# Performance work log

Hardware: AMD Instinct MI355X
Metric: run time of the kernel (lower is better)

The kernel has to match this reference:

```python
import jax, jax.numpy as jnp
import numpy as np

N = 50000
E = 800000
F_IN = 128
H = 128
C = 16


def _balanced_conv(x, row, col, W, b, num_nodes):
    # x: [N, in] -> linear -> gather(row) * norm -> scatter-add(col) + bias
    x = x @ W  # [N, out]
    deg = jax.ops.segment_sum(jnp.ones(row.shape[0], x.dtype), col,
                              num_segments=num_nodes)  # includes self-loops -> deg >= 1
    dinv = deg ** -0.5
    norm = dinv[row] * dinv[col]  # [E+N]
    msg = norm[:, None] * x[row]  # gather + scale
    out = jax.ops.segment_sum(msg, col, num_segments=num_nodes)  # scatter-add
    return out + b


def setup_inputs() -> dict:
    key = jax.random.key(0)
    ks = jax.random.split(key, 12)
    x = jax.random.normal(ks[0], (N, F_IN), dtype=jnp.float32)
    edge_index = jax.random.randint(ks[1], (2, E), 0, N, dtype=jnp.int64)
    s = 1.0 / np.sqrt(F_IN)
    sh = 1.0 / np.sqrt(H)
    return {
        "x": x,
        "edge_index": edge_index,
        "importance": jnp.ones((F_IN,), jnp.float32),
        "W1": jax.random.uniform(ks[2], (F_IN, H), jnp.float32, -s, s),
        "b1": jnp.zeros((H,), jnp.float32),
        "W2": jax.random.uniform(ks[3], (H, H), jnp.float32, -sh, sh),
        "b2": jnp.zeros((H,), jnp.float32),
        "W3": jax.random.uniform(ks[4], (H, H), jnp.float32, -sh, sh),
        "b3": jnp.zeros((H,), jnp.float32),
        "lw1": jax.random.uniform(ks[5], (H, H), jnp.float32, -sh, sh),
        "lb1": jax.random.uniform(ks[6], (H,), jnp.float32, -sh, sh),
        "lw2": jax.random.uniform(ks[7], (H, C), jnp.float32, -sh, sh),
        "lb2": jax.random.uniform(ks[8], (C,), jnp.float32, -sh, sh),
    }


def reference(x, edge_index, importance, W1, b1, W2, b2, W3, b3, lw1, lb1, lw2, lb2):
    num_nodes = x.shape[0]
    # add self-loops (static shape: E + N)
    loops = jnp.arange(num_nodes, dtype=edge_index.dtype)
    row = jnp.concatenate([edge_index[0], loops])
    col = jnp.concatenate([edge_index[1], loops])

    gelu = lambda t: jax.nn.gelu(t, approximate=False)  # torch F.gelu default = erf

    h = x * importance  # FeatureImportance
    h = gelu(_balanced_conv(h, row, col, W1, b1, num_nodes))
    h = gelu(_balanced_conv(h, row, col, W2, b2, num_nodes))
    h = gelu(_balanced_conv(h, row, col, W3, b3, num_nodes))
    h = gelu(h @ lw1 + lb1)
    return h @ lw2 + lb2  # [N, C]
```

## Files before the change

### kernel.cpp

```cpp
#include <hip/hip_runtime.h>
#include <math.h>

#define NNODES 50000
#define NEDGES 800000
#define FDIM 128
#define NBUCKET 196
#define BCAP 6144
#define ABLK 261
#define EPWA 3072
#define MGRID 782

typedef unsigned short ushortT;
typedef unsigned int uintT;
typedef __attribute__((ext_vector_type(8))) short short8;
typedef __attribute__((ext_vector_type(4))) float floatx4;

__device__ __forceinline__ float gelu_erf(float x){
    return 0.5f * x * (1.0f + erff(x * 0.70710678118654752f));
}
__device__ __forceinline__ float bflo(uintT u){ return __uint_as_float(u << 16); }
__device__ __forceinline__ float bfhi(uintT u){ return __uint_as_float(u & 0xFFFF0000u); }
__device__ __forceinline__ ushortT f2bf(float f){
    uintT u = __float_as_uint(f);
    return (ushortT)((u + 0x7FFFu + ((u >> 16) & 1u)) >> 16);
}
__device__ __forceinline__ void split_bf16(float f, ushortT& hi, ushortT& lo){
    uintT u = __float_as_uint(f);
    hi = (ushortT)(u >> 16);
    float fhi = __uint_as_float(u & 0xFFFF0000u);
    lo = (ushortT)(__float_as_uint(f - fhi) >> 16);
}

__global__ __launch_bounds__(256) void k_packW(const float* __restrict__ Wa,
                                               const float* __restrict__ Wb,
                                               const float* __restrict__ Wc,
                                               const float* __restrict__ Wd,
                                               const float* __restrict__ We,
                                               ushortT* __restrict__ Wp,
                                               int* __restrict__ gcur){
    int l = blockIdx.x;
    int t = threadIdx.x;
    if (l < 4){
        const float* W = (l==0) ? Wa : (l==1) ? Wb : (l==2) ? Wc : Wd;
        ushortT* hiP = Wp + (size_t)l*2*16384;
        ushortT* loP = hiP + 16384;
        for (int idx = t; idx < 16384; idx += 256){
            int k = idx >> 7, n = idx & 127;
            ushortT hi, lo;
            split_bf16(W[idx], hi, lo);
            int kc = k >> 5, quad = (k >> 3) & 3, j = k & 7;
            int nt = n >> 4, lane = (n & 15) + (quad << 4);
            int off = ((kc*8 + nt)*64 + lane)*8 + j;
            hiP[off] = hi;
            loP[off] = lo;
        }
    } else {
        if (t < NBUCKET) gcur[t] = 0;
        ushortT* hiP = Wp + (size_t)4*2*16384;
        ushortT* loP = hiP + 2048;
        for (int idx = t; idx < 2048; idx += 256){
            int k = idx >> 4, n = idx & 15;
            ushortT hi, lo;
            split_bf16(We[idx], hi, lo);
            int kc = k >> 5, quad = (k >> 3) & 3, j = k & 7;
            int lane = n + (quad << 4);
            int off = (kc*64 + lane)*8 + j;
            hiP[off] = hi;
            loP[off] = lo;
        }
    }
}

__global__ __launch_bounds__(256) void k_bucketA(const int* __restrict__ ei,
                                                 int* __restrict__ gcur,
                                                 uintT* __restrict__ bucket){
    __shared__ int hist[NBUCKET];
    __shared__ int base[NBUCKET];
    int t = threadIdx.x;
    if (t < NBUCKET) hist[t] = 0;
    __syncthreads();
    int e0 = blockIdx.x * EPWA;
    int cr_c[12], cr_r[12];
    #pragma unroll
    for (int p = 0; p < 12; p++){
        int e = e0 + p*256 + t;
        if (e < NEDGES){
            cr_r[p] = ei[e];
            cr_c[p] = ei[NEDGES + e];
            atomicAdd(&hist[cr_c[p] >> 8], 1);
        } else cr_c[p] = -1;
    }
    __syncthreads();
    if (t < NBUCKET){
        base[t] = atomicAdd(&gcur[t], hist[t]);
        hist[t] = 0;
    }
    __syncthreads();
    #pragma unroll
    for (int p = 0; p < 12; p++){
        int c = cr_c[p];
        if (c >= 0){
            int b = c >> 8;
            int lp = atomicAdd(&hist[b], 1);
            bucket[(size_t)b*BCAP + base[b] + lp] = ((uintT)c << 16) | (uintT)cr_r[p];
        }
    }
}

__global__ __launch_bounds__(256) void k_bucketB(const int* __restrict__ gcur,
                                                 const uintT* __restrict__ bucket,
                                                 int* __restrict__ offs,
                                                 float* __restrict__ dinv,
                                                 ushortT* __restrict__ csr2){
    __shared__ int sm[256];
    __shared__ int hist[256];
    __shared__ int lcur[256];
    int b = blockIdx.x;
    int t = threadIdx.x;
    int n0 = b << 8;

    int gv = (t < NBUCKET) ? gcur[t] : 0;
    sm[t] = gv;
    __syncthreads();
    for (int off = 1; off < 256; off <<= 1){
        int tv = (t >= off) ? sm[t-off] : 0;
        __syncthreads();
        sm[t] += tv;
        __syncthreads();
    }
    __shared__ int bbase_s;
    if (t == b) bbase_s = sm[t] - gv;
    hist[t] = 0;
    __syncthreads();
    int bbase = bbase_s;
    int count = gcur[b];
    const uintT* src = bucket + (size_t)b*BCAP;

    for (int i = t; i < count; i += 256)
        atomicAdd(&hist[(src[i] >> 16) & 255], 1);
    __syncthreads();

    int v = hist[t];
    sm[t] = v;
    __syncthreads();
    for (int off = 1; off < 256; off <<= 1){
        int tv = (t >= off) ? sm[t-off] : 0;
        __syncthreads();
        sm[t] += tv;
        __syncthreads();
    }
    int excl = bbase + sm[t] - v;
    int node = n0 + t;
    if (node <= NNODES) offs[node] = excl;
    if (node < NNODES) dinv[node] = rsqrtf((float)(v + 1));
    if (b == NBUCKET-1 && t == 255) offs[NNODES] = NEDGES;
    lcur[t] = excl;
    __syncthreads();

    for (int i = t; i < count; i += 256){
        uintT e = src[i];
        int pos = atomicAdd(&lcur[(e >> 16) & 255], 1);
        csr2[pos] = (ushortT)(e & 0xFFFFu);
    }
}

__global__ __launch_bounds__(256) void k_mfma_f32(const float* __restrict__ A,
                                                  const ushortT* __restrict__ Wp,
                                                  const float* __restrict__ scale,
                                                  const float* __restrict__ dinv,
                                                  ushortT* __restrict__ Yb){
    __shared__ float As[64*132];
    int t = threadIdx.x;
    int wave = t >> 6, lane = t & 63;
    int r = lane & 15, quad = lane >> 4;
    int row0 = blockIdx.x*64;
    int m0 = row0 + wave*16;
    const ushortT* WpLo = Wp + 16384;

    #pragma unroll
    for (int p = 0; p < 8; p++){
        int idx = p*256 + t;
        int rr = idx >> 5;
        int c4 = idx & 31;
        int gr = row0 + rr;
        float4 v = make_float4(0.f,0.f,0.f,0.f);
        if (gr < NNODES) v = *(const float4*)&A[(size_t)gr*FDIM + c4*4];
        float4 s = *(const float4*)&scale[c4*4];
        v.x*=s.x; v.y*=s.y; v.z*=s.z; v.w*=s.w;
        *(float4*)&As[rr*132 + c4*4] = v;
    }
    __syncthreads();

    floatx4 acc[8];
    #pragma unroll
    for (int nt = 0; nt < 8; nt++) acc[nt] = (floatx4){0.f,0.f,0.f,0.f};

    int arl = wave*16 + r;
    #pragma unroll
    for (int kc = 0; kc < 4; kc++){
        int kb = kc*32 + quad*8;
        float4 a0 = *(const float4*)&As[arl*132 + kb];
        float4 a1 = *(const float4*)&As[arl*132 + kb + 4];
        float av[8] = {a0.x, a0.y, a0.z, a0.w, a1.x, a1.y, a1.z, a1.w};
        short8 ahi, alo;
        #pragma unroll
        for (int e = 0; e < 8; e++){
            ushortT h, l;
            split_bf16(av[e], h, l);
            ahi[e] = (short)h;
            alo[e] = (short)l;
        }
        #pragma unroll
        for (int nt = 0; nt < 8; nt++){
            size_t boff = (size_t)(((kc*8 + nt)*64 + lane))*8;
            short8 bhi = *(const short8*)&Wp[boff];
            short8 blo = *(const short8*)&WpLo[boff];
            acc[nt] = __builtin_amdgcn_mfma_f32_16x16x32_bf16(ahi, bhi, acc[nt], 0, 0, 0);
            acc[nt] = __builtin_amdgcn_mfma_f32_16x16x32_bf16(alo, bhi, acc[nt], 0, 0, 0);
            acc[nt] = __builtin_amdgcn_mfma_f32_16x16x32_bf16(ahi, blo, acc[nt], 0, 0, 0);
        }
    }

    int orow0 = m0 + quad*4;
    float4 dv = *(const float4*)&dinv[orow0];
    float dva[4] = {dv.x, dv.y, dv.z, dv.w};
    #pragma unroll
    for (int nt = 0; nt < 8; nt++){
        int n = nt*16 + r;
        int chunk = n >> 6, o = n & 63;
        #pragma unroll
        for (int reg = 0; reg < 4; reg++){
            int orow = orow0 + reg;
            if (orow < NNODES){
                float v = acc[nt][reg] * dva[reg];
                Yb[((size_t)chunk*NNODES + orow)*64 + o] = f2bf(v);
            }
        }
    }
}

__global__ __launch_bounds__(256) void k_mfma_b16(const ushortT* __restrict__ Ab,
                                                  const ushortT* __restrict__ Wp,
                                                  const float* __restrict__ dinv,
                                                  ushortT* __restrict__ Yb){
    int t = threadIdx.x;
    int wave = t >> 6, lane = t & 63;
    int r = lane & 15, quad = lane >> 4;
    int m0 = blockIdx.x*64 + wave*16;
    int arow = m0 + r;
    if (arow >= NNODES) arow = NNODES - 1;
    const ushortT* WpLo = Wp + 16384;

    floatx4 acc[8];
    #pragma unroll
    for (int nt = 0; nt < 8; nt++) acc[nt] = (floatx4){0.f,0.f,0.f,0.f};

    short8 afr[4];
    #pragma unroll
    for (int kc = 0; kc < 4; kc++)
        afr[kc] = *(const short8*)&Ab[(size_t)arow*FDIM + kc*32 + quad*8];

    #pragma unroll
    for (int kc = 0; kc < 4; kc++){
        #pragma unroll
        for (int nt = 0; nt < 8; nt++){
            size_t boff = (size_t)(((kc*8 + nt)*64 + lane))*8;
            short8 bhi = *(const short8*)&Wp[boff];
            short8 blo = *(const short8*)&WpLo[boff];
            acc[nt] = __builtin_amdgcn_mfma_f32_16x16x32_bf16(afr[kc], bhi, acc[nt], 0, 0, 0);
            acc[nt] = __builtin_amdgcn_mfma_f32_16x16x32_bf16(afr[kc], blo, acc[nt], 0, 0, 0);
        }
    }

    int orow0 = m0 + quad*4;
    float4 dv = *(const float4*)&dinv[orow0];
    float dva[4] = {dv.x, dv.y, dv.z, dv.w};
    #pragma unroll
    for (int nt = 0; nt < 8; nt++){
        int n = nt*16 + r;
        int chunk = n >> 6, o = n & 63;
        #pragma unroll
        for (int reg = 0; reg < 4; reg++){
            int orow = orow0 + reg;
            if (orow < NNODES){
                float v = acc[nt][reg] * dva[reg];
                Yb[((size_t)chunk*NNODES + orow)*64 + o] = f2bf(v);
            }
        }
    }
}

__global__ __launch_bounds__(256) void k_mfma_final(const ushortT* __restrict__ Ab,
                                                    const ushortT* __restrict__ Wp1,
                                                    const ushortT* __restrict__ Wp2,
                                                    const float* __restrict__ lb1,
                                                    const float* __restrict__ lb2,
                                                    float* __restrict__ out){
    __shared__ ushortT Ls[64*136];
    int t = threadIdx.x;
    int wave = t >> 6, lane = t & 63;
    int r = lane & 15, quad = lane >> 4;
    int row0 = blockIdx.x*64;
    int m0 = row0 + wave*16;
    int arow = m0 + r;
    if (arow >= NNODES) arow = NNODES - 1;
    const ushortT* Wp1Lo = Wp1 + 16384;
    const ushortT* Wp2Lo = Wp2 + 2048;

    floatx4 acc[8];
    #pragma unroll
    for (int nt = 0; nt < 8; nt++) acc[nt] = (floatx4){0.f,0.f,0.f,0.f};

    short8 afr[4];
    #pragma unroll
    for (int kc = 0; kc < 4; kc++)
        afr[kc] = *(const short8*)&Ab[(size_t)arow*FDIM + kc*32 + quad*8];

    #pragma unroll
    for (int kc = 0; kc < 4; kc++){
        #pragma unroll
        for (int nt = 0; nt < 8; nt++){
            size_t boff = (size_t)(((kc*8 + nt)*64 + lane))*8;
            short8 bhi = *(const short8*)&Wp1[boff];
            short8 blo = *(const short8*)&Wp1Lo[boff];
            acc[nt] = __builtin_amdgcn_mfma_f32_16x16x32_bf16(afr[kc], bhi, acc[nt], 0, 0, 0);
            acc[nt] = __builtin_amdgcn_mfma_f32_16x16x32_bf16(afr[kc], blo, acc[nt], 0, 0, 0);
        }
    }

    int lrow0 = wave*16 + quad*4;
    #pragma unroll
    for (int nt = 0; nt < 8; nt++){
        int n = nt*16 + r;
        float bv = lb1[n];
        #pragma unroll
        for (int reg = 0; reg < 4; reg++){
            Ls[(lrow0 + reg)*136 + n] = f2bf(gelu_erf(acc[nt][reg] + bv));
        }
    }
    __syncthreads();

    floatx4 acc2 = (floatx4){0.f,0.f,0.f,0.f};
    #pragma unroll
    for (int kc = 0; kc < 4; kc++){
        short8 a2 = *(const short8*)&Ls[(wave*16 + r)*136 + kc*32 + quad*8];
        short8 bhi = *(const short8*)&Wp2[(size_t)(kc*64 + lane)*8];
        short8 blo = *(const short8*)&Wp2Lo[(size_t)(kc*64 + lane)*8];
        acc2 = __builtin_amdgcn_mfma_f32_16x16x32_bf16(a2, bhi, acc2, 0, 0, 0);
        acc2 = __builtin_amdgcn_mfma_f32_16x16x32_bf16(a2, blo, acc2, 0, 0, 0);
    }
    float bv2 = lb2[r];
    #pragma unroll
    for (int reg = 0; reg < 4; reg++){
        int orow = m0 + quad*4 + reg;
        if (orow < NNODES)
            out[(size_t)orow*16 + r] = acc2[reg] + bv2;
    }
}

__global__ __launch_bounds__(256) void k_aggregate(const ushortT* __restrict__ Yt,
                                                   const float* __restrict__ dinv,
                                                   const int* __restrict__ offs,
                                                   const ushortT* __restrict__ csr2,
                                                   const float* __restrict__ bias,
                                                   ushortT* __restrict__ Hout){
    int bid = blockIdx.x;
    int chunk = bid & 1;
    int node = (bid >> 1) * 8 + (threadIdx.x >> 5);
    int lane = threadIdx.x & 31;
    const uintT* Yc = (const uintT*)Yt + (size_t)chunk * NNODES * 32;

    uintT a0 = Yc[node*32 + lane];
    float2 acc;
    acc.x = bflo(a0);
    acc.y = bfhi(a0);
    int e0 = offs[node], e1 = offs[node+1];
    int e = e0;
    for (; e + 7 < e1; e += 8){
        int r0 = csr2[e+0];
        int r1 = csr2[e+1];
        int r2 = csr2[e+2];
        int r3 = csr2[e+3];
        int r4 = csr2[e+4];
        int r5 = csr2[e+5];
        int r6 = csr2[e+6];
        int r7 = csr2[e+7];
        uintT q0 = Yc[r0*32 + lane];
        uintT q1 = Yc[r1*32 + lane];
        uintT q2 = Yc[r2*32 + lane];
        uintT q3 = Yc[r3*32 + lane];
        uintT q4 = Yc[r4*32 + lane];
        uintT q5 = Yc[r5*32 + lane];
        uintT q6 = Yc[r6*32 + lane];
        uintT q7 = Yc[r7*32 + lane];
        acc.x += bflo(q0); acc.y += bfhi(q0);
        acc.x += bflo(q1); acc.y += bfhi(q1);
        acc.x += bflo(q2); acc.y += bfhi(q2);
        acc.x += bflo(q3); acc.y += bfhi(q3);
        acc.x += bflo(q4); acc.y += bfhi(q4);
        acc.x += bflo(q5); acc.y += bfhi(q5);
        acc.x += bflo(q6); acc.y += bfhi(q6);
        acc.x += bflo(q7); acc.y += bfhi(q7);
    }
    for (; e + 1 < e1; e += 2){
        int r0 = csr2[e], r1 = csr2[e+1];
        uintT q0 = Yc[r0*32 + lane];
        uintT q1 = Yc[r1*32 + lane];
        acc.x += bflo(q0); acc.y += bfhi(q0);
        acc.x += bflo(q1); acc.y += bfhi(q1);
    }
    if (e < e1){
        uintT q = Yc[csr2[e]*32 + lane];
        acc.x += bflo(q); acc.y += bfhi(q);
    }
    float dc = dinv[node];
    float2 bv = ((const float2*)bias)[chunk*32 + lane];
    acc.x = gelu_erf(fmaf(dc, acc.x, bv.x));
    acc.y = gelu_erf(fmaf(dc, acc.y, bv.y));
    uintT packed = (uintT)f2bf(acc.x) | ((uintT)f2bf(acc.y) << 16);
    *(uintT*)&Hout[(size_t)node*FDIM + chunk*64 + lane*2] = packed;
}

extern "C" void kernel_launch(void* const* d_in, const int* in_sizes, int n_in,
                              void* d_out, int out_size, void* d_ws, size_t ws_size,
                              hipStream_t stream) {
    const float* x    = (const float*)d_in[0];
    const int*   ei   = (const int*)d_in[1];
    const float* imp  = (const float*)d_in[2];
    const float* W1   = (const float*)d_in[3];
    const float* b1   = (const float*)d_in[4];
    const float* W2   = (const float*)d_in[5];
    const float* b2   = (const float*)d_in[6];
    const float* W3   = (const float*)d_in[7];
    const float* b3   = (const float*)d_in[8];
    const float* lw1  = (const float*)d_in[9];
    const float* lb1  = (const float*)d_in[10];
    const float* lw2  = (const float*)d_in[11];
    const float* lb2  = (const float*)d_in[12];
    float* out = (float*)d_out;

    int*   offs   = (int*)d_ws;
    int*   gcur   = (int*)d_ws + 50048;
    float* dinv   = (float*)d_ws + 50304;
    ushortT* csr2 = (ushortT*)((int*)d_ws + 100480);
    uintT* bucket = (uintT*)((int*)d_ws + 500480);
    ushortT* Wp   = (ushortT*)((int*)d_ws + 1704704);
    ushortT* bufYt= (ushortT*)((int*)d_ws + 1772544);
    ushortT* bufH = (ushortT*)((int*)d_ws + 4972544);

    dim3 B(256);
    k_packW  <<<5, B, 0, stream>>>(W1, W2, W3, lw1, lw2, Wp, gcur);
    k_bucketA<<<ABLK, B, 0, stream>>>(ei, gcur, bucket);
    k_bucketB<<<NBUCKET, B, 0, stream>>>(gcur, bucket, offs, dinv, csr2);

    k_mfma_f32 <<<MGRID, B, 0, stream>>>(x, Wp + 0*32768, imp, dinv, bufYt);
    k_aggregate<<<(NNODES/8)*2, B, 0, stream>>>(bufYt, dinv, offs, csr2, b1, bufH);
    k_mfma_b16 <<<MGRID, B, 0, stream>>>(bufH, Wp + 1*32768, dinv, bufYt);
    k_aggregate<<<(NNODES/8)*2, B, 0, stream>>>(bufYt, dinv, offs, csr2, b2, bufH);
    k_mfma_b16 <<<MGRID, B, 0, stream>>>(bufH, Wp + 2*32768, dinv, bufYt);
    k_aggregate<<<(NNODES/8)*2, B, 0, stream>>>(bufYt, dinv, offs, csr2, b3, bufH);

    k_mfma_final<<<MGRID, B, 0, stream>>>(bufH, Wp + 3*32768, Wp + 4*32768, lb1, lb2, out);
}
```

Before: 318.5 us.

## Fuse neighbor aggregation with following GEMM via shared-memory tile, row-major Y layout

Merges each aggregation kernel with the next layer's MFMA GEMM (and the final MLP). Each block aggregates 64 nodes into LDS and then multiplies from LDS. The intermediate Y layout changes from two 64-column chunks to full row-major 128 columns, so one wave gathers a full 256-byte row per edge. This removes the H round trip through global memory and three launches. In exchange, each block runs only 4 waves with a 16-node serial loop per wave, which lowers parallelism for the latency-bound gather and worsens load imbalance on degree skew.

```diff
diff --git a/kernel.cpp b/kernel.cpp
--- a/kernel.cpp
+++ b/kernel.cpp
@@ -164,6 +164,69 @@
     }
 }
 
+__device__ __forceinline__ void agg_phase(const uintT* __restrict__ Y2,
+                                          const float* __restrict__ dinv,
+                                          const int* __restrict__ offs,
+                                          const ushortT* __restrict__ csr2,
+                                          const float* __restrict__ bias,
+                                          uintT* __restrict__ Hs, int row0,
+                                          int wave, int lane){
+    float2 bv = ((const float2*)bias)[lane];
+    for (int g = 0; g < 16; g++){
+        int lrow = (g << 2) + wave;
+        int node = row0 + lrow;
+        float2 acc = make_float2(0.f, 0.f);
+        float dc = 0.f;
+        if (node < NNODES){
+            dc = dinv[node];
+            uintT a0 = Y2[(size_t)node*64 + lane];
+            acc.x = bflo(a0); acc.y = bfhi(a0);
+            int e0 = offs[node], e1 = offs[node+1];
+            int e = e0;
+            for (; e + 7 < e1; e += 8){
+                int s0 = csr2[e+0];
+                int s1 = csr2[e+1];
+                int s2 = csr2[e+2];
+                int s3 = csr2[e+3];
+                int s4 = csr2[e+4];
+                int s5 = csr2[e+5];
+                int s6 = csr2[e+6];
+                int s7 = csr2[e+7];
+                uintT q0 = Y2[(size_t)s0*64 + lane];
+                uintT q1 = Y2[(size_t)s1*64 + lane];
+                uintT q2 = Y2[(size_t)s2*64 + lane];
+                uintT q3 = Y2[(size_t)s3*64 + lane];
+                uintT q4 = Y2[(size_t)s4*64 + lane];
+                uintT q5 = Y2[(size_t)s5*64 + lane];
+                uintT q6 = Y2[(size_t)s6*64 + lane];
+                uintT q7 = Y2[(size_t)s7*64 + lane];
+                acc.x += bflo(q0); acc.y += bfhi(q0);
+                acc.x += bflo(q1); acc.y += bfhi(q1);
+                acc.x += bflo(q2); acc.y += bfhi(q2);
+                acc.x += bflo(q3); acc.y += bfhi(q3);
+                acc.x += bflo(q4); acc.y += bfhi(q4);
+                acc.x += bflo(q5); acc.y += bfhi(q5);
+                acc.x += bflo(q6); acc.y += bfhi(q6);
+                acc.x += bflo(q7); acc.y += bfhi(q7);
+            }
+            for (; e + 1 < e1; e += 2){
+                int s0 = csr2[e], s1 = csr2[e+1];
+                uintT q0 = Y2[(size_t)s0*64 + lane];
+                uintT q1 = Y2[(size_t)s1*64 + lane];
+                acc.x += bflo(q0); acc.y += bfhi(q0);
+                acc.x += bflo(q1); acc.y += bfhi(q1);
+            }
+            if (e < e1){
+                uintT q = Y2[(size_t)csr2[e]*64 + lane];
+                acc.x += bflo(q); acc.y += bfhi(q);
+            }
+        }
+        float ox = gelu_erf(fmaf(dc, acc.x, bv.x));
+        float oy = gelu_erf(fmaf(dc, acc.y, bv.y));
+        Hs[lrow*66 + lane] = (uintT)f2bf(ox) | ((uintT)f2bf(oy) << 16);
+    }
+}
+
 __global__ __launch_bounds__(256) void k_mfma_f32(const float* __restrict__ A,
                                                   const ushortT* __restrict__ Wp,
                                                   const float* __restrict__ scale,
@@ -227,39 +290,41 @@
     #pragma unroll
     for (int nt = 0; nt < 8; nt++){
         int n = nt*16 + r;
-        int chunk = n >> 6, o = n & 63;
         #pragma unroll
         for (int reg = 0; reg < 4; reg++){
             int orow = orow0 + reg;
-            if (orow < NNODES){
-                float v = acc[nt][reg] * dva[reg];
-                Yb[((size_t)chunk*NNODES + orow)*64 + o] = f2bf(v);
-            }
-        }
-    }
-}
-
-__global__ __launch_bounds__(256) void k_mfma_b16(const ushortT* __restrict__ Ab,
+            if (orow < NNODES)
+                Yb[(size_t)orow*FDIM + n] = f2bf(acc[nt][reg] * dva[reg]);
+        }
+    }
+}
+
+__global__ __launch_bounds__(256) void k_agg_gemm(const uintT* __restrict__ Yin,
+                                                  const float* __restrict__ dinv,
+                                                  const int* __restrict__ offs,
+                                                  const ushortT* __restrict__ csr2,
+                                                  const float* __restrict__ bias,
                                                   const ushortT* __restrict__ Wp,
-                                                  const float* __restrict__ dinv,
-                                                  ushortT* __restrict__ Yb){
+                                                  ushortT* __restrict__ Yout){
+    __shared__ uintT Hs[64*66];
     int t = threadIdx.x;
     int wave = t >> 6, lane = t & 63;
+    int row0 = blockIdx.x*64;
+    agg_phase(Yin, dinv, offs, csr2, bias, Hs, row0, wave, lane);
+    __syncthreads();
+
     int r = lane & 15, quad = lane >> 4;
-    int m0 = blockIdx.x*64 + wave*16;
-    int arow = m0 + r;
-    if (arow >= NNODES) arow = NNODES - 1;
+    const ushortT* HsS = (const ushortT*)Hs;
     const ushortT* WpLo = Wp + 16384;
+    int arl = wave*16 + r;
+    short8 afr[4];
+    #pragma unroll
+    for (int kc = 0; kc < 4; kc++)
+        afr[kc] = *(const short8*)&HsS[arl*132 + kc*32 + quad*8];
 
     floatx4 acc[8];
     #pragma unroll
     for (int nt = 0; nt < 8; nt++) acc[nt] = (floatx4){0.f,0.f,0.f,0.f};
-
-    short8 afr[4];
-    #pragma unroll
-    for (int kc = 0; kc < 4; kc++)
-        afr[kc] = *(const short8*)&Ab[(size_t)arow*FDIM + kc*32 + quad*8];
-
     #pragma unroll
     for (int kc = 0; kc < 4; kc++){
         #pragma unroll
@@ -272,50 +337,53 @@
         }
     }
 
+    int m0 = row0 + wave*16;
     int orow0 = m0 + quad*4;
     float4 dv = *(const float4*)&dinv[orow0];
     float dva[4] = {dv.x, dv.y, dv.z, dv.w};
     #pragma unroll
     for (int nt = 0; nt < 8; nt++){
         int n = nt*16 + r;
-        int chunk = n >> 6, o = n & 63;
         #pragma unroll
         for (int reg = 0; reg < 4; reg++){
             int orow = orow0 + reg;
-            if (orow < NNODES){
-                float v = acc[nt][reg] * dva[reg];
-                Yb[((size_t)chunk*NNODES + orow)*64 + o] = f2bf(v);
-            }
-        }
-    }
-}
-
-__global__ __launch_bounds__(256) void k_mfma_final(const ushortT* __restrict__ Ab,
-                                                    const ushortT* __restrict__ Wp1,
-                                                    const ushortT* __restrict__ Wp2,
-                                                    const float* __restrict__ lb1,
-                                                    const float* __restrict__ lb2,
-                                                    float* __restrict__ out){
-    __shared__ ushortT Ls[64*136];
+            if (orow < NNODES)
+                Yout[(size_t)orow*FDIM + n] = f2bf(acc[nt][reg] * dva[reg]);
+        }
+    }
+}
+
+__global__ __launch_bounds__(256) void k_agg_final(const uintT* __restrict__ Yin,
+                                                   const float* __restrict__ dinv,
+                                                   const int* __restrict__ offs,
+                                                   const ushortT* __restrict__ csr2,
+                                                   const float* __restrict__ bias,
+                                                   const ushortT* __restrict__ Wp1,
+                                                   const ushortT* __restrict__ Wp2,
+                                                   const float* __restrict__ lb1,
+                                                   const float* __restrict__ lb2,
+                                                   float* __restrict__ out){
+    __shared__ uintT Hs[64*66];
+    __shared__ ushortT Ps[64*136];
     int t = threadIdx.x;
     int wave = t >> 6, lane = t & 63;
+    int row0 = blockIdx.x*64;
+    agg_phase(Yin, dinv, offs, csr2, bias, Hs, row0, wave, lane);
+    __syncthreads();
+
     int r = lane & 15, quad = lane >> 4;
-    int row0 = blockIdx.x*64;
-    int m0 = row0 + wave*16;
-    int arow = m0 + r;
-    if (arow >= NNODES) arow = NNODES - 1;
+    const ushortT* HsS = (const ushortT*)Hs;
     const ushortT* Wp1Lo = Wp1 + 16384;
     const ushortT* Wp2Lo = Wp2 + 2048;
+    int arl = wave*16 + r;
+    short8 afr[4];
+    #pragma unroll
+    for (int kc = 0; kc < 4; kc++)
+        afr[kc] = *(const short8*)&HsS[arl*132 + kc*32 + quad*8];
 
     floatx4 acc[8];
     #pragma unroll
     for (int nt = 0; nt < 8; nt++) acc[nt] = (floatx4){0.f,0.f,0.f,0.f};
-
-    short8 afr[4];
-    #pragma unroll
-    for (int kc = 0; kc < 4; kc++)
-        afr[kc] = *(const short8*)&Ab[(size_t)arow*FDIM + kc*32 + quad*8];
-
     #pragma unroll
     for (int kc = 0; kc < 4; kc++){
         #pragma unroll
@@ -334,91 +402,28 @@
         int n = nt*16 + r;
         float bv = lb1[n];
         #pragma unroll
-        for (int reg = 0; reg < 4; reg++){
-            Ls[(lrow0 + reg)*136 + n] = f2bf(gelu_erf(acc[nt][reg] + bv));
-        }
+        for (int reg = 0; reg < 4; reg++)
+            Ps[(lrow0 + reg)*136 + n] = f2bf(gelu_erf(acc[nt][reg] + bv));
     }
     __syncthreads();
 
     floatx4 acc2 = (floatx4){0.f,0.f,0.f,0.f};
     #pragma unroll
     for (int kc = 0; kc < 4; kc++){
-        short8 a2 = *(const short8*)&Ls[(wave*16 + r)*136 + kc*32 + quad*8];
+        short8 a2 = *(const short8*)&Ps[(wave*16 + r)*136 + kc*32 + quad*8];
         short8 bhi = *(const short8*)&Wp2[(size_t)(kc*64 + lane)*8];
         short8 blo = *(const short8*)&Wp2Lo[(size_t)(kc*64 + lane)*8];
         acc2 = __builtin_amdgcn_mfma_f32_16x16x32_bf16(a2, bhi, acc2, 0, 0, 0);
         acc2 = __builtin_amdgcn_mfma_f32_16x16x32_bf16(a2, blo, acc2, 0, 0, 0);
     }
     float bv2 = lb2[r];
+    int m0 = row0 + wave*16;
     #pragma unroll
     for (int reg = 0; reg < 4; reg++){
         int orow = m0 + quad*4 + reg;
         if (orow < NNODES)
             out[(size_t)orow*16 + r] = acc2[reg] + bv2;
     }
-}
-
-__global__ __launch_bounds__(256) void k_aggregate(const ushortT* __restrict__ Yt,
-                                                   const float* __restrict__ dinv,
-                                                   const int* __restrict__ offs,
-                                                   const ushortT* __restrict__ csr2,
-                                                   const float* __restrict__ bias,
-                                                   ushortT* __restrict__ Hout){
-    int bid = blockIdx.x;
-    int chunk = bid & 1;
-    int node = (bid >> 1) * 8 + (threadIdx.x >> 5);
-    int lane = threadIdx.x & 31;
-    const uintT* Yc = (const uintT*)Yt + (size_t)chunk * NNODES * 32;
-
-    uintT a0 = Yc[node*32 + lane];
-    float2 acc;
-    acc.x = bflo(a0);
-    acc.y = bfhi(a0);
-    int e0 = offs[node], e1 = offs[node+1];
-    int e = e0;
-    for (; e + 7 < e1; e += 8){
-        int r0 = csr2[e+0];
-        int r1 = csr2[e+1];
-        int r2 = csr2[e+2];
-        int r3 = csr2[e+3];
-        int r4 = csr2[e+4];
-        int r5 = csr2[e+5];
-        int r6 = csr2[e+6];
-        int r7 = csr2[e+7];
-        uintT q0 = Yc[r0*32 + lane];
-        uintT q1 = Yc[r1*32 + lane];
-        uintT q2 = Yc[r2*32 + lane];
-        uintT q3 = Yc[r3*32 + lane];
-        uintT q4 = Yc[r4*32 + lane];
-        uintT q5 = Yc[r5*32 + lane];
-        uintT q6 = Yc[r6*32 + lane];
-        uintT q7 = Yc[r7*32 + lane];
-        acc.x += bflo(q0); acc.y += bfhi(q0);
-        acc.x += bflo(q1); acc.y += bfhi(q1);
-        acc.x += bflo(q2); acc.y += bfhi(q2);
-        acc.x += bflo(q3); acc.y += bfhi(q3);
-        acc.x += bflo(q4); acc.y += bfhi(q4);
-        acc.x += bflo(q5); acc.y += bfhi(q5);
-        acc.x += bflo(q6); acc.y += bfhi(q6);
-        acc.x += bflo(q7); acc.y += bfhi(q7);
-    }
-    for (; e + 1 < e1; e += 2){
-        int r0 = csr2[e], r1 = csr2[e+1];
-        uintT q0 = Yc[r0*32 + lane];
-        uintT q1 = Yc[r1*32 + lane];
-        acc.x += bflo(q0); acc.y += bfhi(q0);
-        acc.x += bflo(q1); acc.y += bfhi(q1);
-    }
-    if (e < e1){
-        uintT q = Yc[csr2[e]*32 + lane];
-        acc.x += bflo(q); acc.y += bfhi(q);
-    }
-    float dc = dinv[node];
-    float2 bv = ((const float2*)bias)[chunk*32 + lane];
-    acc.x = gelu_erf(fmaf(dc, acc.x, bv.x));
-    acc.y = gelu_erf(fmaf(dc, acc.y, bv.y));
-    uintT packed = (uintT)f2bf(acc.x) | ((uintT)f2bf(acc.y) << 16);
-    *(uintT*)&Hout[(size_t)node*FDIM + chunk*64 + lane*2] = packed;
 }
 
 extern "C" void kernel_launch(void* const* d_in, const int* in_sizes, int n_in,
@@ -445,20 +450,17 @@
     ushortT* csr2 = (ushortT*)((int*)d_ws + 100480);
     uintT* bucket = (uintT*)((int*)d_ws + 500480);
     ushortT* Wp   = (ushortT*)((int*)d_ws + 1704704);
-    ushortT* bufYt= (ushortT*)((int*)d_ws + 1772544);
-    ushortT* bufH = (ushortT*)((int*)d_ws + 4972544);
+    uintT* bufY0  = (uintT*)((int*)d_ws + 1772288);
+    uintT* bufY1  = (uintT*)((int*)d_ws + 4976288);
 
     dim3 B(256);
     k_packW  <<<5, B, 0, stream>>>(W1, W2, W3, lw1, lw2, Wp, gcur);
     k_bucketA<<<ABLK, B, 0, stream>>>(ei, gcur, bucket);
     k_bucketB<<<NBUCKET, B, 0, stream>>>(gcur, bucket, offs, dinv, csr2);
 
-    k_mfma_f32 <<<MGRID, B, 0, stream>>>(x, Wp + 0*32768, imp, dinv, bufYt);
-    k_aggregate<<<(NNODES/8)*2, B, 0, stream>>>(bufYt, dinv, offs, csr2, b1, bufH);
-    k_mfma_b16 <<<MGRID, B, 0, stream>>>(bufH, Wp + 1*32768, dinv, bufYt);
-    k_aggregate<<<(NNODES/8)*2, B, 0, stream>>>(bufYt, dinv, offs, csr2, b2, bufH);
-    k_mfma_b16 <<<MGRID, B, 0, stream>>>(bufH, Wp + 2*32768, dinv, bufYt);
-    k_aggregate<<<(NNODES/8)*2, B, 0, stream>>>(bufYt, dinv, offs, csr2, b3, bufH);
-
-    k_mfma_final<<<MGRID, B, 0, stream>>>(bufH, Wp + 3*32768, Wp + 4*32768, lb1, lb2, out);
-}
+    k_mfma_f32<<<MGRID, B, 0, stream>>>(x, Wp + 0*32768, imp, dinv, (ushortT*)bufY0);
+    k_agg_gemm<<<MGRID, B, 0, stream>>>(bufY0, dinv, offs, csr2, b1, Wp + 1*32768, (ushortT*)bufY1);
+    k_agg_gemm<<<MGRID, B, 0, stream>>>(bufY1, dinv, offs, csr2, b2, Wp + 2*32768, (ushortT*)bufY0);
+    k_agg_final<<<MGRID, B, 0, stream>>>(bufY0, dinv, offs, csr2, b3,
+                                         Wp + 3*32768, Wp + 4*32768, lb1, lb2, out);
+}
```

Result: slower. 341.1 us (+7.1%).

## Store transformed features row-major and gather full 128-wide rows per node

Applied to the files above, without the earlier changes.

The GEMM epilogues now write Y as plain row-major [N,128] bf16 instead of two 64-column chunk planes. The aggregation kernel processes the whole 128-feature row per node, with each of 32 lanes loading 8 bytes (4 bf16). That halves the number of blocks and the repeated CSR index reads. Each gathered neighbour row becomes one 256-byte contiguous access instead of two 128-byte accesses in separate planes, at the cost of losing the chunked layout's smaller per-plane working set for cache locality.

```diff
diff --git a/kernel.cpp b/kernel.cpp
--- a/kernel.cpp
+++ b/kernel.cpp
@@ -227,14 +227,11 @@
     #pragma unroll
     for (int nt = 0; nt < 8; nt++){
         int n = nt*16 + r;
-        int chunk = n >> 6, o = n & 63;
         #pragma unroll
         for (int reg = 0; reg < 4; reg++){
             int orow = orow0 + reg;
-            if (orow < NNODES){
-                float v = acc[nt][reg] * dva[reg];
-                Yb[((size_t)chunk*NNODES + orow)*64 + o] = f2bf(v);
-            }
+            if (orow < NNODES)
+                Yb[(size_t)orow*FDIM + n] = f2bf(acc[nt][reg] * dva[reg]);
         }
     }
 }
@@ -278,14 +275,11 @@
     #pragma unroll
     for (int nt = 0; nt < 8; nt++){
         int n = nt*16 + r;
-        int chunk = n >> 6, o = n & 63;
         #pragma unroll
         for (int reg = 0; reg < 4; reg++){
             int orow = orow0 + reg;
-            if (orow < NNODES){
-                float v = acc[nt][reg] * dva[reg];
-                Yb[((size_t)chunk*NNODES + orow)*64 + o] = f2bf(v);
-            }
+            if (orow < NNODES)
+                Yb[(size_t)orow*FDIM + n] = f2bf(acc[nt][reg] * dva[reg]);
         }
     }
 }
@@ -334,9 +328,8 @@
         int n = nt*16 + r;
         float bv = lb1[n];
         #pragma unroll
-        for (int reg = 0; reg < 4; reg++){
+        for (int reg = 0; reg < 4; reg++)
             Ls[(lrow0 + reg)*136 + n] = f2bf(gelu_erf(acc[nt][reg] + bv));
-        }
     }
     __syncthreads();
 
@@ -358,67 +351,69 @@
     }
 }
 
-__global__ __launch_bounds__(256) void k_aggregate(const ushortT* __restrict__ Yt,
+__global__ __launch_bounds__(256) void k_aggregate(const uintT* __restrict__ Y2,
                                                    const float* __restrict__ dinv,
                                                    const int* __restrict__ offs,
                                                    const ushortT* __restrict__ csr2,
                                                    const float* __restrict__ bias,
                                                    ushortT* __restrict__ Hout){
-    int bid = blockIdx.x;
-    int chunk = bid & 1;
-    int node = (bid >> 1) * 8 + (threadIdx.x >> 5);
+    int node = blockIdx.x*8 + (threadIdx.x >> 5);
     int lane = threadIdx.x & 31;
-    const uintT* Yc = (const uintT*)Yt + (size_t)chunk * NNODES * 32;
-
-    uintT a0 = Yc[node*32 + lane];
-    float2 acc;
-    acc.x = bflo(a0);
-    acc.y = bfhi(a0);
+    const uint2* Yu = (const uint2*)Y2;
+
+    uint2 a0 = Yu[(size_t)node*32 + lane];
+    float4 acc;
+    acc.x = bflo(a0.x); acc.y = bfhi(a0.x);
+    acc.z = bflo(a0.y); acc.w = bfhi(a0.y);
     int e0 = offs[node], e1 = offs[node+1];
     int e = e0;
     for (; e + 7 < e1; e += 8){
-        int r0 = csr2[e+0];
-        int r1 = csr2[e+1];
-        int r2 = csr2[e+2];
-        int r3 = csr2[e+3];
-        int r4 = csr2[e+4];
-        int r5 = csr2[e+5];
-        int r6 = csr2[e+6];
-        int r7 = csr2[e+7];
-        uintT q0 = Yc[r0*32 + lane];
-        uintT q1 = Yc[r1*32 + lane];
-        uintT q2 = Yc[r2*32 + lane];
-        uintT q3 = Yc[r3*32 + lane];
-        uintT q4 = Yc[r4*32 + lane];
-        uintT q5 = Yc[r5*32 + lane];
-        uintT q6 = Yc[r6*32 + lane];
-        uintT q7 = Yc[r7*32 + lane];
-        acc.x += bflo(q0); acc.y += bfhi(q0);
-        acc.x += bflo(q1); acc.y += bfhi(q1);
-        acc.x += bflo(q2); acc.y += bfhi(q2);
-        acc.x += bflo(q3); acc.y += bfhi(q3);
-        acc.x += bflo(q4); acc.y += bfhi(q4);
-        acc.x += bflo(q5); acc.y += bfhi(q5);
-        acc.x += bflo(q6); acc.y += bfhi(q6);
-        acc.x += bflo(q7); acc.y += bfhi(q7);
+        int s0 = csr2[e+0];
+        int s1 = csr2[e+1];
+        int s2 = csr2[e+2];
+        int s3 = csr2[e+3];
+        int s4 = csr2[e+4];
+        int s5 = csr2[e+5];
+        int s6 = csr2[e+6];
+        int s7 = csr2[e+7];
+        uint2 q0 = Yu[(size_t)s0*32 + lane];
+        uint2 q1 = Yu[(size_t)s1*32 + lane];
+        uint2 q2 = Yu[(size_t)s2*32 + lane];
+        uint2 q3 = Yu[(size_t)s3*32 + lane];
+        uint2 q4 = Yu[(size_t)s4*32 + lane];
+        uint2 q5 = Yu[(size_t)s5*32 + lane];
+        uint2 q6 = Yu[(size_t)s6*32 + lane];
+        uint2 q7 = Yu[(size_t)s7*32 + lane];
+        acc.x += bflo(q0.x); acc.y += bfhi(q0.x); acc.z += bflo(q0.y); acc.w += bfhi(q0.y);
+        acc.x += bflo(q1.x); acc.y += bfhi(q1.x); acc.z += bflo(q1.y); acc.w += bfhi(q1.y);
+        acc.x += bflo(q2.x); acc.y += bfhi(q2.x); acc.z += bflo(q2.y); acc.w += bfhi(q2.y);
+        acc.x += bflo(q3.x); acc.y += bfhi(q3.x); acc.z += bflo(q3.y); acc.w += bfhi(q3.y);
+        acc.x += bflo(q4.x); acc.y += bfhi(q4.x); acc.z += bflo(q4.y); acc.w += bfhi(q4.y);
+        acc.x += bflo(q5.x); acc.y += bfhi(q5.x); acc.z += bflo(q5.y); acc.w += bfhi(q5.y);
+        acc.x += bflo(q6.x); acc.y += bfhi(q6.x); acc.z += bflo(q6.y); acc.w += bfhi(q6.y);
+        acc.x += bflo(q7.x); acc.y += bfhi(q7.x); acc.z += bflo(q7.y); acc.w += bfhi(q7.y);
     }
     for (; e + 1 < e1; e += 2){
-        int r0 = csr2[e], r1 = csr2[e+1];
-        uintT q0 = Yc[r0*32 + lane];
-        uintT q1 = Yc[r1*32 + lane];
-        acc.x += bflo(q0); acc.y += bfhi(q0);
-        acc.x += bflo(q1); acc.y += bfhi(q1);
+        int s0 = csr2[e], s1 = csr2[e+1];
+        uint2 q0 = Yu[(size_t)s0*32 + lane];
+        uint2 q1 = Yu[(size_t)s1*32 + lane];
+        acc.x += bflo(q0.x); acc.y += bfhi(q0.x); acc.z += bflo(q0.y); acc.w += bfhi(q0.y);
+        acc.x += bflo(q1.x); acc.y += bfhi(q1.x); acc.z += bflo(q1.y); acc.w += bfhi(q1.y);
     }
     if (e < e1){
-        uintT q = Yc[csr2[e]*32 + lane];
-        acc.x += bflo(q); acc.y += bfhi(q);
+        uint2 q = Yu[(size_t)csr2[e]*32 + lane];
+        acc.x += bflo(q.x); acc.y += bfhi(q.x); acc.z += bflo(q.y); acc.w += bfhi(q.y);
     }
     float dc = dinv[node];
-    float2 bv = ((const float2*)bias)[chunk*32 + lane];
+    float4 bv = ((const float4*)bias)[lane];
     acc.x = gelu_erf(fmaf(dc, acc.x, bv.x));
     acc.y = gelu_erf(fmaf(dc, acc.y, bv.y));
-    uintT packed = (uintT)f2bf(acc.x) | ((uintT)f2bf(acc.y) << 16);
-    *(uintT*)&Hout[(size_t)node*FDIM + chunk*64 + lane*2] = packed;
+    acc.z = gelu_erf(fmaf(dc, acc.z, bv.z));
+    acc.w = gelu_erf(fmaf(dc, acc.w, bv.w));
+    uint2 o;
+    o.x = (uintT)f2bf(acc.x) | ((uintT)f2bf(acc.y) << 16);
+    o.y = (uintT)f2bf(acc.z) | ((uintT)f2bf(acc.w) << 16);
+    *(uint2*)&Hout[(size_t)node*FDIM + lane*4] = o;
 }
 
 extern "C" void kernel_launch(void* const* d_in, const int* in_sizes, int n_in,
@@ -445,20 +440,20 @@
     ushortT* csr2 = (ushortT*)((int*)d_ws + 100480);
     uintT* bucket = (uintT*)((int*)d_ws + 500480);
     ushortT* Wp   = (ushortT*)((int*)d_ws + 1704704);
-    ushortT* bufYt= (ushortT*)((int*)d_ws + 1772544);
-    ushortT* bufH = (ushortT*)((int*)d_ws + 4972544);
+    uintT* bufY   = (uintT*)((int*)d_ws + 1772288);
+    ushortT* bufH = (ushortT*)((int*)d_ws + 4972288);
 
     dim3 B(256);
     k_packW  <<<5, B, 0, stream>>>(W1, W2, W3, lw1, lw2, Wp, gcur);
     k_bucketA<<<ABLK, B, 0, stream>>>(ei, gcur, bucket);
     k_bucketB<<<NBUCKET, B, 0, stream>>>(gcur, bucket, offs, dinv, csr2);
 
-    k_mfma_f32 <<<MGRID, B, 0, stream>>>(x, Wp + 0*32768, imp, dinv, bufYt);
-    k_aggregate<<<(NNODES/8)*2, B, 0, stream>>>(bufYt, dinv, offs, csr2, b1, bufH);
-    k_mfma_b16 <<<MGRID, B, 0, stream>>>(bufH, Wp + 1*32768, dinv, bufYt);
-    k_aggregate<<<(NNODES/8)*2, B, 0, stream>>>(bufYt, dinv, offs, csr2, b2, bufH);
-    k_mfma_b16 <<<MGRID, B, 0, stream>>>(bufH, Wp + 2*32768, dinv, bufYt);
-    k_aggregate<<<(NNODES/8)*2, B, 0, stream>>>(bufYt, dinv, offs, csr2, b3, bufH);
+    k_mfma_f32 <<<MGRID, B, 0, stream>>>(x, Wp + 0*32768, imp, dinv, (ushortT*)bufY);
+    k_aggregate<<<NNODES/8, B, 0, stream>>>(bufY, dinv, offs, csr2, b1, bufH);
+    k_mfma_b16 <<<MGRID, B, 0, stream>>>(bufH, Wp + 1*32768, dinv, (ushortT*)bufY);
+    k_aggregate<<<NNODES/8, B, 0, stream>>>(bufY, dinv, offs, csr2, b2, bufH);
+    k_mfma_b16 <<<MGRID, B, 0, stream>>>(bufH, Wp + 2*32768, dinv, (ushortT*)bufY);
+    k_aggregate<<<NNODES/8, B, 0, stream>>>(bufY, dinv, offs, csr2, b3, bufH);
 
     k_mfma_final<<<MGRID, B, 0, stream>>>(bufH, Wp + 3*32768, Wp + 4*32768, lb1, lb2, out);
 }
```

Result: faster. 300.9 us (-5.5%).
